# Optimization experiments

Hardware: AMD Instinct MI355X
Metric: run time of the kernel (lower is better)

Reference implementation:

```python
import jax, jax.numpy as jnp
import numpy as np

IN_CH, OUT_CH, L, INTERVAL = 128, 128, 80, 5
NCPT = int(np.ceil(L / INTERVAL)) + 1            # 17 anchor points
INTERVAL2 = 1 if INTERVAL == 1 else L - (NCPT - 2) * INTERVAL  # 5
P = (L + 1) ** 2                                  # 6561 positions
# static repeat_interleave index: degree l occupies 2l+1 positions
REPEAT_IDX = np.repeat(np.arange(L + 1), 2 * np.arange(L + 1) + 1)  # [P]


def setup_inputs() -> dict:
    key = jax.random.key(0)
    kx, kw = jax.random.split(key)
    x = jax.random.normal(kx, (16, IN_CH, P), dtype=jnp.float32)
    stdv = 1.0 / float(np.sqrt(IN_CH * (L + 1)))
    weight = jax.random.uniform(kw, (IN_CH, OUT_CH, NCPT, 1), dtype=jnp.float32,
                                minval=-stdv, maxval=stdv)
    return {"x": x, "weight": weight}


def _interp_filter(weight):
    # weight: [in, out, ncpt, 1] -> per-degree coeffs [in, out, L+1]
    w = weight[..., 0]                                   # [in, out, ncpt]
    l0 = jnp.arange(INTERVAL, dtype=w.dtype) / INTERVAL  # [interval]
    # segments between anchors 0..ncpt-2: [in, out, ncpt-2, interval]
    w1 = (1.0 - l0) * w[:, :, :-2, None] + l0 * w[:, :, 1:-1, None]
    w1 = w1.reshape(w.shape[0], w.shape[1], -1)          # [in, out, (ncpt-2)*interval]
    l1 = jnp.arange(INTERVAL2 + 1, dtype=w.dtype) / INTERVAL2  # [interval2+1]
    w2 = (1.0 - l1) * w[:, :, -2, None] + l1 * w[:, :, -1, None]  # [in, out, interval2+1]
    wl = jnp.concatenate([w1, w2], axis=2)               # [in, out, L+1]
    return wl[:, :, REPEAT_IDX]                          # [in, out, P]


def reference(x, weight):
    wp = _interp_filter(weight)                          # [in, out, P]
    # out[b,o,p] = sum_i wp[i,o,p] * x[b,i,p]  (fused, no [b,in,out,P] temp)
    return jnp.einsum('iop,bip->bop', wp, x)
```

## Files before the change

kernel.cpp:

```cpp
#include <hip/hip_runtime.h>

#define IC    128
#define OC    128
#define LMAX  80
#define NL    81
#define PTOT  6561
#define NCPT  17
#define BSTR  (IC*PTOT)
#define NBLK  1681

typedef short short8 __attribute__((ext_vector_type(8)));
typedef float f32x4  __attribute__((ext_vector_type(4)));

__device__ __forceinline__ unsigned short f2bf(float x) {
    unsigned u = __float_as_uint(x);
    return (unsigned short)((u + 0x7FFFu + ((u >> 16) & 1u)) >> 16);
}

__global__ __launch_bounds__(256) void shconv_prep(const float* __restrict__ w,
                                                   unsigned short* __restrict__ Wt) {
    const int o = blockIdx.x;
    const int t = threadIdx.x;
    __shared__ float ws[IC * NCPT];
    for (int e = t; e < IC * NCPT; e += 256) {
        int i = e / NCPT;
        int s = e - i * NCPT;
        ws[e] = w[i * (OC * NCPT) + o * NCPT + s];
    }
    __syncthreads();
    for (int f = t; f < NL * IC; f += 256) {
        int l = f >> 7;
        int i = f & 127;
        int s; float fr;
        if (l < 75) { s = l / 5;  fr = (float)(l - s * 5) / 5.0f; }
        else        { s = 15;     fr = (float)(l - 75) / 5.0f;    }
        float v = (1.0f - fr) * ws[i * NCPT + s] + fr * ws[i * NCPT + s + 1];
        Wt[l * (OC * IC) + o * IC + i] = f2bf(v);
    }
}

__global__ __launch_bounds__(256) void shconv_main(const float* __restrict__ x,
                                                   const unsigned short* __restrict__ Wt,
                                                   float* __restrict__ out) {
    __shared__ __align__(16) unsigned short Wl[128 * 136];

    const int tid = threadIdx.x;

    int q = blockIdx.x;
    int t = (int)sqrtf((float)q);
    while (t * t > q) --t;
    while ((t + 1) * (t + 1) <= q) ++t;
    int l, chunk;
    if (q < t * (t + 1)) { l = 2 * t - 1; chunk = q - t * t; }
    else                 { l = 2 * t;     chunk = q - t * (t + 1); }

    const int len  = 2 * l + 1;
    const int cols = 16 * len;
    const int c0   = chunk * 64;

    {
        const unsigned short* src = Wt + l * (OC * IC);
        #pragma unroll
        for (int it = 0; it < 8; ++it) {
            int idx = tid + it * 256;
            int o   = idx >> 4;
            int seg = idx & 15;
            *(uint4*)(&Wl[o * 136 + seg * 8]) = *(const uint4*)(src + idx * 8);
        }
    }
    __syncthreads();

    const int lane = tid & 63;
    const int wave = tid >> 6;
    const int m    = lane & 15;
    const int g    = lane >> 4;

    int c = c0 + wave * 16 + m;
    const bool valid = (c < cols);
    int ccl = valid ? c : (cols - 1);
    int b   = (int)((unsigned)ccl / (unsigned)len);
    int pp  = ccl - b * len;
    int p   = l * l + pp;

    const float* xg = x + (size_t)b * BSTR + (size_t)(g * 8) * PTOT + p;

    float xv[32];
    #pragma unroll
    for (int kk = 0; kk < 4; ++kk)
        #pragma unroll
        for (int j = 0; j < 8; ++j)
            xv[kk * 8 + j] = xg[(kk * 32 + j) * PTOT];

    short8 bfr[4];
    #pragma unroll
    for (int kk = 0; kk < 4; ++kk)
        #pragma unroll
        for (int j = 0; j < 8; ++j)
            bfr[kk][j] = (short)f2bf(xv[kk * 8 + j]);

    f32x4 acc[8];
    #pragma unroll
    for (int of = 0; of < 8; ++of) acc[of] = (f32x4){0.f, 0.f, 0.f, 0.f};

    #pragma unroll
    for (int kk = 0; kk < 4; ++kk) {
        #pragma unroll
        for (int of = 0; of < 8; ++of) {
            short8 af = *(const short8*)(&Wl[(of * 16 + m) * 136 + kk * 32 + g * 8]);
            acc[of] = __builtin_amdgcn_mfma_f32_16x16x32_bf16(af, bfr[kk], acc[of], 0, 0, 0);
        }
    }

    if (valid) {
        float* ob = out + (size_t)b * (OC * PTOT) + p;
        #pragma unroll
        for (int of = 0; of < 8; ++of)
            #pragma unroll
            for (int j = 0; j < 4; ++j)
                ob[(of * 16 + g * 4 + j) * PTOT] = acc[of][j];
    }
}

extern "C" void kernel_launch(void* const* d_in, const int* in_sizes, int n_in,
                              void* d_out, int out_size, void* d_ws, size_t ws_size,
                              hipStream_t stream) {
    const float* x = (const float*)d_in[0];
    const float* w = (const float*)d_in[1];
    unsigned short* Wt = (unsigned short*)d_ws;
    float* out = (float*)d_out;

    shconv_prep<<<dim3(OC), dim3(256), 0, stream>>>(w, Wt);
    shconv_main<<<dim3(NBLK), dim3(256), 0, stream>>>(x, Wt, out);
}
```

Measured before the change: 136.9 us.

## Pre-swizzle weights into MFMA fragment order and drop LDS staging

```diff
diff --git a/kernel.cpp b/kernel.cpp
--- a/kernel.cpp
+++ b/kernel.cpp
@@ -2,7 +2,6 @@
 
 #define IC    128
 #define OC    128
-#define LMAX  80
 #define NL    81
 #define PTOT  6561
 #define NCPT  17
@@ -18,32 +17,29 @@
 }
 
 __global__ __launch_bounds__(256) void shconv_prep(const float* __restrict__ w,
-                                                   unsigned short* __restrict__ Wt) {
-    const int o = blockIdx.x;
-    const int t = threadIdx.x;
-    __shared__ float ws[IC * NCPT];
-    for (int e = t; e < IC * NCPT; e += 256) {
-        int i = e / NCPT;
-        int s = e - i * NCPT;
-        ws[e] = w[i * (OC * NCPT) + o * NCPT + s];
-    }
-    __syncthreads();
-    for (int f = t; f < NL * IC; f += 256) {
-        int l = f >> 7;
-        int i = f & 127;
-        int s; float fr;
-        if (l < 75) { s = l / 5;  fr = (float)(l - s * 5) / 5.0f; }
-        else        { s = 15;     fr = (float)(l - 75) / 5.0f;    }
-        float v = (1.0f - fr) * ws[i * NCPT + s] + fr * ws[i * NCPT + s + 1];
-        Wt[l * (OC * IC) + o * IC + i] = f2bf(v);
+                                                   unsigned short* __restrict__ WtF) {
+    const int l = blockIdx.x;
+    int s; float fr;
+    if (l < 75) { s = l / 5;  fr = (float)(l - s * 5) * 0.2f; }
+    else        { s = 15;     fr = (float)(l - 75) * 0.2f;    }
+    unsigned short* dst = WtF + (size_t)l * (OC * IC);
+    for (int e = threadIdx.x; e < OC * IC; e += 256) {
+        int j  = e & 7;
+        int mm = (e >> 3) & 15;
+        int gg = (e >> 7) & 3;
+        int kk = (e >> 9) & 3;
+        int of = e >> 11;
+        int o = of * 16 + mm;
+        int i = kk * 32 + gg * 8 + j;
+        const float* wp = w + i * (OC * NCPT) + o * NCPT + s;
+        float v = (1.0f - fr) * wp[0] + fr * wp[1];
+        dst[e] = f2bf(v);
     }
 }
 
 __global__ __launch_bounds__(256) void shconv_main(const float* __restrict__ x,
-                                                   const unsigned short* __restrict__ Wt,
+                                                   const unsigned short* __restrict__ WtF,
                                                    float* __restrict__ out) {
-    __shared__ __align__(16) unsigned short Wl[128 * 136];
-
     const int tid = threadIdx.x;
 
     int q = blockIdx.x;
@@ -58,18 +54,6 @@
     const int cols = 16 * len;
     const int c0   = chunk * 64;
 
-    {
-        const unsigned short* src = Wt + l * (OC * IC);
-        #pragma unroll
-        for (int it = 0; it < 8; ++it) {
-            int idx = tid + it * 256;
-            int o   = idx >> 4;
-            int seg = idx & 15;
-            *(uint4*)(&Wl[o * 136 + seg * 8]) = *(const uint4*)(src + idx * 8);
-        }
-    }
-    __syncthreads();
-
     const int lane = tid & 63;
     const int wave = tid >> 6;
     const int m    = lane & 15;
@@ -83,6 +67,7 @@
     int p   = l * l + pp;
 
     const float* xg = x + (size_t)b * BSTR + (size_t)(g * 8) * PTOT + p;
+    const unsigned short* wf = WtF + (size_t)l * (OC * IC) + (size_t)lane * 8;
 
     float xv[32];
     #pragma unroll
@@ -106,7 +91,7 @@
     for (int kk = 0; kk < 4; ++kk) {
         #pragma unroll
         for (int of = 0; of < 8; ++of) {
-            short8 af = *(const short8*)(&Wl[(of * 16 + m) * 136 + kk * 32 + g * 8]);
+            short8 af = *(const short8*)(wf + (size_t)(of * 4 + kk) * 512);
             acc[of] = __builtin_amdgcn_mfma_f32_16x16x32_bf16(af, bfr[kk], acc[of], 0, 0, 0);
         }
     }
@@ -126,9 +111,9 @@
                               hipStream_t stream) {
     const float* x = (const float*)d_in[0];
     const float* w = (const float*)d_in[1];
-    unsigned short* Wt = (unsigned short*)d_ws;
+    unsigned short* WtF = (unsigned short*)d_ws;
     float* out = (float*)d_out;
 
-    shconv_prep<<<dim3(OC), dim3(256), 0, stream>>>(w, Wt);
-    shconv_main<<<dim3(NBLK), dim3(256), 0, stream>>>(x, Wt, out);
+    shconv_prep<<<dim3(NL),   dim3(256), 0, stream>>>(w, WtF);
+    shconv_main<<<dim3(NBLK), dim3(256), 0, stream>>>(x, WtF, out);
 }
```

Measured after the change: 147.7 us. +7.9%, slower.
